# Performance work log

Hardware: AMD Instinct MI355X
Metric: run time of the kernel (lower is better)

The kernel has to match this reference:

```python
import jax, jax.numpy as jnp
import numpy as np
import math

B, T_TOK, D, H, L, V, NC, BS = 8, 511, 768, 12, 8, 512, 10, 512

PARAM_NAMES = ['tok_emb','cond_emb','type_emb','pos_emb','ln1_g','ln1_b','Wq','bq','Wk','bk','Wv','bv','Wp','bp','ln2_g','ln2_b','W1','b1','W2','b2','lnf_g','lnf_b','head_w']


def setup_inputs() -> dict:
    key = jax.random.key(0)
    ks = iter(jax.random.split(key, 40))
    def w(shape):
        return jax.random.normal(next(ks), shape, jnp.float32) * 0.02
    inp = {
        'idx': jax.random.randint(next(ks), (B, T_TOK), 0, V),
        'condition': jax.random.randint(next(ks), (B,), 0, NC + 1),
        'tok_emb': w((V, D)),
        'cond_emb': w((NC + 1, D)),
        'type_emb': w((2, D)),
        'pos_emb': w((1, BS, D)),
        'ln1_g': jnp.ones((L, D)), 'ln1_b': jnp.zeros((L, D)),
        'Wq': w((L, D, D)), 'bq': jnp.zeros((L, D)),
        'Wk': w((L, D, D)), 'bk': jnp.zeros((L, D)),
        'Wv': w((L, D, D)), 'bv': jnp.zeros((L, D)),
        'Wp': w((L, D, D)), 'bp': jnp.zeros((L, D)),
        'ln2_g': jnp.ones((L, D)), 'ln2_b': jnp.zeros((L, D)),
        'W1': w((L, D, 4 * D)), 'b1': jnp.zeros((L, 4 * D)),
        'W2': w((L, 4 * D, D)), 'b2': jnp.zeros((L, D)),
        'lnf_g': jnp.ones((D,)), 'lnf_b': jnp.zeros((D,)),
        'head_w': w((D, V)),
    }
    return inp


def _ln(x, g, b):
    m = x.mean(-1, keepdims=True)
    v = ((x - m) ** 2).mean(-1, keepdims=True)
    return (x - m) * jax.lax.rsqrt(v + 1e-5) * g + b


def _forward(idx, condition, p):
    b, t = idx.shape
    T = t + 1  # conditioning token prepended
    x = jnp.concatenate([p['cond_emb'][condition][:, None, :], p['tok_emb'][idx]], axis=1)
    type_ids = jnp.concatenate([jnp.zeros((1,), jnp.int32), jnp.ones((t,), jnp.int32)])
    x = x + p['pos_emb'][:, :T] + p['type_emb'][type_ids][None]
    dh = D // H
    causal = jnp.tril(jnp.ones((T, T), bool))

    def block(x, lp):
        ln1_g, ln1_b, Wq, bq, Wk, bk, Wv, bv, Wp, bp, ln2_g, ln2_b, W1, b1, W2, b2 = lp
        h = _ln(x, ln1_g, ln1_b)
        def heads(W, bias):
            return (h @ W + bias).reshape(b, T, H, dh).transpose(0, 2, 1, 3)  # [b,H,T,dh]
        q, k, v = heads(Wq, bq), heads(Wk, bk), heads(Wv, bv)
        att = jnp.einsum('bhqd,bhkd->bhqk', q, k) * (1.0 / math.sqrt(dh))
        att = jax.nn.softmax(jnp.where(causal, att, -jnp.inf), axis=-1)
        y = jnp.einsum('bhqk,bhkd->bhqd', att, v).transpose(0, 2, 1, 3).reshape(b, T, D)
        # NOTE: original Block applies ln1 in-place, so residual base is post-ln h
        x = h + (y @ Wp + bp)
        h2 = _ln(x, ln2_g, ln2_b)
        x = x + (jax.nn.gelu(h2 @ W1 + b1, approximate=False) @ W2 + b2)
        return x, None

    lp = (p['ln1_g'], p['ln1_b'], p['Wq'], p['bq'], p['Wk'], p['bk'], p['Wv'], p['bv'],
          p['Wp'], p['bp'], p['ln2_g'], p['ln2_b'], p['W1'], p['b1'], p['W2'], p['b2'])
    x, _ = jax.lax.scan(block, x, lp)
    logits = _ln(x, p['lnf_g'], p['lnf_b']) @ p['head_w']
    return logits[:, 1:, :]  # strip conditioning position (cond_len=1)


def reference(idx, condition, tok_emb, cond_emb, type_emb, pos_emb, ln1_g, ln1_b, Wq, bq, Wk, bk, Wv, bv, Wp, bp, ln2_g, ln2_b, W1, b1, W2, b2, lnf_g, lnf_b, head_w):
    p = dict(zip(PARAM_NAMES, (tok_emb, cond_emb, type_emb, pos_emb, ln1_g, ln1_b, Wq, bq, Wk, bk, Wv, bv, Wp, bp, ln2_g, ln2_b, W1, b1, W2, b2, lnf_g, lnf_b, head_w)))
    return _forward(idx, condition, p)
```

## Files before the change

kernel.cpp:

```cpp
#include <hip/hip_runtime.h>
#include <hip/hip_bf16.h>
#include <cstddef>
#include <cstdint>


#define NTOK 4096
#define TSEQ 512
#define DMODEL 768
#define DFF 3072
#define NHEAD 12
#define DHEAD 64
#define NLAYER 8
#define VOCAB 512
#define QKVD 2304

typedef __attribute__((ext_vector_type(8))) __bf16 bf16x8;
typedef __attribute__((ext_vector_type(4))) float f32x4;
typedef __attribute__((ext_vector_type(4))) unsigned int u32x4;
typedef __attribute__((ext_vector_type(4))) unsigned short u16x4;

__device__ __forceinline__ unsigned short f2bf(float f) {
  union { float f; unsigned int u; } v; v.f = f;
  return (unsigned short)((v.u + 0x7FFFu + ((v.u >> 16) & 1u)) >> 16);
}

__device__ __forceinline__ float gelu_exact(float x) {
  return 0.5f * x * (1.f + erff(x * 0.70710678118654752f));
}

__device__ __forceinline__ void gload_lds16(const void* g, void* lds) {
  __builtin_amdgcn_global_load_lds(
      reinterpret_cast<__attribute__((address_space(1))) void*>(
          reinterpret_cast<uintptr_t>(g)),
      reinterpret_cast<__attribute__((address_space(3))) void*>(
          reinterpret_cast<uintptr_t>(lds)),
      16, 0, 0);
}

__global__ __launch_bounds__(256) void embed_k(
    const int* __restrict__ idx, const int* __restrict__ cond,
    const float* __restrict__ tok, const float* __restrict__ ce,
    const float* __restrict__ te, const float* __restrict__ pe,
    float* __restrict__ X) {
  int row = blockIdx.x;
  int b = row >> 9, t = row & 511;
  int tid = threadIdx.x;
  const float* src = (t == 0) ? (ce + (size_t)cond[b] * DMODEL)
                              : (tok + (size_t)idx[b * 511 + t - 1] * DMODEL);
  const float* ty = te + (t != 0 ? DMODEL : 0);
  const float* pp = pe + (size_t)t * DMODEL;
  float* dst = X + (size_t)row * DMODEL;
#pragma unroll
  for (int i = 0; i < 3; i++) {
    int d = tid + i * 256;
    dst[d] = src[d] + pp[d] + ty[d];
  }
}

template <bool F32OUT>
__global__ __launch_bounds__(256) void ln_k(
    const float* __restrict__ X, const float* __restrict__ g,
    const float* __restrict__ bta, float* __restrict__ O,
    unsigned short* __restrict__ Ob) {
  const int row = blockIdx.x;
  const int tid = threadIdx.x;
  const float* x = X + (size_t)row * DMODEL;
  float v0 = x[tid], v1 = x[tid + 256], v2 = x[tid + 512];
  float s = v0 + v1 + v2;
  float ss = v0 * v0 + v1 * v1 + v2 * v2;
#pragma unroll
  for (int o = 32; o > 0; o >>= 1) {
    s += __shfl_down(s, o);
    ss += __shfl_down(ss, o);
  }
  __shared__ float sm[8];
  const int wid = tid >> 6, lane = tid & 63;
  if (lane == 0) { sm[wid] = s; sm[wid + 4] = ss; }
  __syncthreads();
  float st = sm[0] + sm[1] + sm[2] + sm[3];
  float sst = sm[4] + sm[5] + sm[6] + sm[7];
  float mean = st * (1.f / DMODEL);
  float var = sst * (1.f / DMODEL) - mean * mean;
  float rstd = rsqrtf(var + 1e-5f);
  float y0 = (v0 - mean) * rstd * g[tid] + bta[tid];
  float y1 = (v1 - mean) * rstd * g[tid + 256] + bta[tid + 256];
  float y2 = (v2 - mean) * rstd * g[tid + 512] + bta[tid + 512];
  if (F32OUT) {
    float* o = O + (size_t)row * DMODEL;
    o[tid] = y0; o[tid + 256] = y1; o[tid + 512] = y2;
  }
  unsigned short* ob = Ob + (size_t)row * DMODEL;
  ob[tid] = f2bf(y0); ob[tid + 256] = f2bf(y1); ob[tid + 512] = f2bf(y2);
}

struct P4 { const float* p[4]; };

__global__ __launch_bounds__(256) void transp_k(P4 src,
                                                unsigned short* __restrict__ out,
                                                int K, int N) {
  __shared__ float Ls[64][65];
  const float* W = src.p[blockIdx.z];
  unsigned short* o = out + (size_t)blockIdx.z * K * N;
  const int tid = threadIdx.x;
  const int n0 = blockIdx.x * 64, k0 = blockIdx.y * 64;
  const int r = tid >> 4, c4 = (tid & 15) * 4;
#pragma unroll
  for (int i = 0; i < 4; i++) {
    const int kk = r + i * 16;
    const float4 v = *(const float4*)(W + (size_t)(k0 + kk) * N + n0 + c4);
    Ls[c4 + 0][kk] = v.x;
    Ls[c4 + 1][kk] = v.y;
    Ls[c4 + 2][kk] = v.z;
    Ls[c4 + 3][kk] = v.w;
  }
  __syncthreads();
#pragma unroll
  for (int i = 0; i < 4; i++) {
    const int nn = r + i * 16;
    u16x4 q;
    q.x = f2bf(Ls[nn][c4 + 0]);
    q.y = f2bf(Ls[nn][c4 + 1]);
    q.z = f2bf(Ls[nn][c4 + 2]);
    q.w = f2bf(Ls[nn][c4 + 3]);
    *(u16x4*)(o + (size_t)(n0 + nn) * K + k0 + c4) = q;
  }
}

__global__ __launch_bounds__(256) void packb_k(const float* __restrict__ bq,
                                               const float* __restrict__ bk,
                                               const float* __restrict__ bv,
                                               float* __restrict__ o) {
  const int l = blockIdx.x, tid = threadIdx.x;
#pragma unroll
  for (int i = 0; i < 9; i++) {
    int n = tid + i * 256;
    float v = (n < 768) ? bq[l * 768 + n]
                        : (n < 1536) ? bk[l * 768 + n - 768]
                                     : bv[l * 768 + n - 1536];
    o[l * QKVD + n] = v;
  }
}

#define BK 32

constexpr int EPQ = 0;
constexpr int EPRES = 1;
constexpr int EPGELU = 2;
constexpr int EPHEAD = 3;
constexpr int EPQB = 4;

template <int EP, int TBM, int TBN>
__global__ __launch_bounds__(256) void mm_k(
    const unsigned short* __restrict__ A, const unsigned short* __restrict__ Bt,
    const float* __restrict__ bias, const float* __restrict__ res,
    void* __restrict__ Cv, int K, int N) {
  __shared__ unsigned short As[TBM * BK];
  __shared__ unsigned short Bs[TBN * BK];
  constexpr int WM = TBM / 2, WN = TBN / 2;
  constexpr int MI = WM / 16, NJ = WN / 16;
  const int tid = threadIdx.x;
  const int lane = tid & 63, wid = tid >> 6;
  const int wr = wid >> 1, wc = wid & 1;
  const int m0 = blockIdx.x * TBM, n0 = blockIdx.y * TBN;

  f32x4 acc[MI][NJ];
#pragma unroll
  for (int i = 0; i < MI; i++)
#pragma unroll
    for (int j = 0; j < NJ; j++) acc[i][j] = f32x4{0.f, 0.f, 0.f, 0.f};

  const int srow = lane >> 2;
  const int gch = (lane & 3) ^ (srow & 3);
  const size_t rb = (size_t)K * 2;
  const int fr = lane & 15, ks = lane >> 4;

  for (int k0 = 0; k0 < K; k0 += BK) {
#pragma unroll
    for (int t = 0; t < TBM / 64; t++) {
      const int rr = wid * (TBM / 4) + t * 16;
      gload_lds16((const char*)A + (size_t)(m0 + rr + srow) * rb +
                      (size_t)k0 * 2 + gch * 16,
                  As + rr * BK);
    }
#pragma unroll
    for (int t = 0; t < TBN / 64; t++) {
      const int rr = wid * (TBN / 4) + t * 16;
      gload_lds16((const char*)Bt + (size_t)(n0 + rr + srow) * rb +
                      (size_t)k0 * 2 + gch * 16,
                  Bs + rr * BK);
    }
    __syncthreads();

    u32x4 ar[MI], br[NJ];
#pragma unroll
    for (int i = 0; i < MI; i++) {
      const int ra = wr * WM + i * 16 + fr;
      ar[i] = *(const u32x4*)((const char*)As + ra * 64 + ((ks ^ (ra & 3)) << 4));
    }
#pragma unroll
    for (int j = 0; j < NJ; j++) {
      const int rbw = wc * WN + j * 16 + fr;
      br[j] = *(const u32x4*)((const char*)Bs + rbw * 64 + ((ks ^ (rbw & 3)) << 4));
    }
#pragma unroll
    for (int i = 0; i < MI; i++)
#pragma unroll
      for (int j = 0; j < NJ; j++)
        acc[i][j] = __builtin_amdgcn_mfma_f32_16x16x32_bf16(
            __builtin_bit_cast(bf16x8, ar[i]), __builtin_bit_cast(bf16x8, br[j]),
            acc[i][j], 0, 0, 0);
    __syncthreads();
  }

#pragma unroll
  for (int i = 0; i < MI; i++) {
#pragma unroll
    for (int j = 0; j < NJ; j++) {
      const int n = n0 + wc * WN + j * 16 + fr;
      float bv = 0.f;
      if (EP != EPHEAD) bv = bias[n];
#pragma unroll
      for (int r = 0; r < 4; r++) {
        const int m = m0 + wr * WM + i * 16 + ks * 4 + r;
        float v = acc[i][j][r] + bv;
        if (EP == EPRES) v += res[(size_t)m * N + n];
        if (EP == EPGELU) {
          ((unsigned short*)Cv)[(size_t)m * N + n] = f2bf(gelu_exact(v));
        } else if (EP == EPQB) {
          ((unsigned short*)Cv)[(size_t)m * N + n] = f2bf(v);
        } else if (EP == EPHEAD) {
          const int bb = m >> 9, tt = m & 511;
          if (tt)
            ((float*)Cv)[(size_t)(bb * 511 + tt - 1) * N + n] = v;
        } else {
          ((float*)Cv)[(size_t)m * N + n] = v;
        }
      }
    }
  }
}

__global__ __launch_bounds__(256) void attn_mfma_k(
    const unsigned short* __restrict__ QKV, unsigned short* __restrict__ Y) {
  __shared__ unsigned short Ks[64][72];
  __shared__ unsigned short Vt[64][72];
  __shared__ unsigned short Pl[4][16][72];
  const int qt = 7 - (int)blockIdx.x;
  const int h = blockIdx.y, b = blockIdx.z;
  const int tid = threadIdx.x;
  const int lane = tid & 63, wq = tid >> 6;
  const int fr = lane & 15, g = lane >> 4;

  const size_t qrow =
      (size_t)(b * TSEQ + qt * 64 + wq * 16 + fr) * QKVD + h * DHEAD;
  u32x4 qf[2];
  qf[0] = *(const u32x4*)(QKV + qrow + g * 8);
  qf[1] = *(const u32x4*)(QKV + qrow + 32 + g * 8);

  f32x4 of[4];
  float m[4], l[4];
#pragma unroll
  for (int jd = 0; jd < 4; jd++) of[jd] = f32x4{0.f, 0.f, 0.f, 0.f};
#pragma unroll
  for (int r = 0; r < 4; r++) { m[r] = -1e30f; l[r] = 0.f; }

  const int srow = tid >> 2, sc = (tid & 3) * 16;

  for (int kt = 0; kt <= qt; kt++) {
    {
      const size_t kr = (size_t)(b * TSEQ + kt * 64 + srow) * QKVD + h * DHEAD;
      u32x4 k0 = *(const u32x4*)(QKV + kr + DMODEL + sc);
      u32x4 k1 = *(const u32x4*)(QKV + kr + DMODEL + sc + 8);
      *(u32x4*)&Ks[srow][sc] = k0;
      *(u32x4*)&Ks[srow][sc + 8] = k1;
      u32x4 v0 = *(const u32x4*)(QKV + kr + 2 * DMODEL + sc);
      u32x4 v1 = *(const u32x4*)(QKV + kr + 2 * DMODEL + sc + 8);
      const unsigned short* vp = (const unsigned short*)&v0;
#pragma unroll
      for (int i = 0; i < 8; i++) Vt[sc + i][srow] = vp[i];
      vp = (const unsigned short*)&v1;
#pragma unroll
      for (int i = 0; i < 8; i++) Vt[sc + 8 + i][srow] = vp[i];
    }
    __syncthreads();

    f32x4 sf[4];
#pragma unroll
    for (int j = 0; j < 4; j++) sf[j] = f32x4{0.f, 0.f, 0.f, 0.f};
#pragma unroll
    for (int st = 0; st < 2; st++) {
#pragma unroll
      for (int j = 0; j < 4; j++) {
        u32x4 kf = *(const u32x4*)&Ks[j * 16 + fr][st * 32 + g * 8];
        sf[j] = __builtin_amdgcn_mfma_f32_16x16x32_bf16(
            __builtin_bit_cast(bf16x8, qf[st]), __builtin_bit_cast(bf16x8, kf),
            sf[j], 0, 0, 0);
      }
    }

    const bool diag = (kt == qt);
#pragma unroll
    for (int r = 0; r < 4; r++) {
      float pv[4];
      float mx = -1e30f;
#pragma unroll
      for (int j = 0; j < 4; j++) {
        float sv = sf[j][r] * 0.125f;
        if (diag && (j * 16 + fr > wq * 16 + g * 4 + r)) sv = -1e30f;
        pv[j] = sv;
        mx = fmaxf(mx, sv);
      }
      mx = fmaxf(mx, __shfl_xor(mx, 1));
      mx = fmaxf(mx, __shfl_xor(mx, 2));
      mx = fmaxf(mx, __shfl_xor(mx, 4));
      mx = fmaxf(mx, __shfl_xor(mx, 8));
      const float mn = fmaxf(m[r], mx);
      const float corr = __expf(m[r] - mn);
      m[r] = mn;
      float ls = 0.f;
#pragma unroll
      for (int j = 0; j < 4; j++) {
        const float e = __expf(pv[j] - mn);
        Pl[wq][g * 4 + r][j * 16 + fr] = f2bf(e);
        ls += e;
      }
      ls += __shfl_xor(ls, 1);
      ls += __shfl_xor(ls, 2);
      ls += __shfl_xor(ls, 4);
      ls += __shfl_xor(ls, 8);
      l[r] = l[r] * corr + ls;
#pragma unroll
      for (int jd = 0; jd < 4; jd++) of[jd][r] *= corr;
    }

#pragma unroll
    for (int st = 0; st < 2; st++) {
      u32x4 pf = *(const u32x4*)&Pl[wq][fr][st * 32 + g * 8];
#pragma unroll
      for (int jd = 0; jd < 4; jd++) {
        u32x4 vf = *(const u32x4*)&Vt[jd * 16 + fr][st * 32 + g * 8];
        of[jd] = __builtin_amdgcn_mfma_f32_16x16x32_bf16(
            __builtin_bit_cast(bf16x8, pf), __builtin_bit_cast(bf16x8, vf),
            of[jd], 0, 0, 0);
      }
    }
    __syncthreads();
  }

#pragma unroll
  for (int r = 0; r < 4; r++) {
    const float inv = 1.f / l[r];
    const size_t orow =
        (size_t)(b * TSEQ + qt * 64 + wq * 16 + g * 4 + r) * DMODEL + h * DHEAD;
#pragma unroll
    for (int jd = 0; jd < 4; jd++)
      Y[orow + jd * 16 + fr] = f2bf(of[jd][r] * inv);
  }
}

extern "C" void kernel_launch(void* const* d_in, const int* in_sizes, int n_in,
                              void* d_out, int out_size, void* d_ws, size_t ws_size,
                              hipStream_t stream) {
  const int* idx = (const int*)d_in[0];
  const int* condition = (const int*)d_in[1];
  const float* tok_emb = (const float*)d_in[2];
  const float* cond_emb = (const float*)d_in[3];
  const float* type_emb = (const float*)d_in[4];
  const float* pos_emb = (const float*)d_in[5];
  const float* ln1_g = (const float*)d_in[6];
  const float* ln1_b = (const float*)d_in[7];
  const float* Wq = (const float*)d_in[8];
  const float* bq = (const float*)d_in[9];
  const float* Wk = (const float*)d_in[10];
  const float* bk = (const float*)d_in[11];
  const float* Wv = (const float*)d_in[12];
  const float* bv = (const float*)d_in[13];
  const float* Wp = (const float*)d_in[14];
  const float* bp = (const float*)d_in[15];
  const float* ln2_g = (const float*)d_in[16];
  const float* ln2_b = (const float*)d_in[17];
  const float* W1 = (const float*)d_in[18];
  const float* b1 = (const float*)d_in[19];
  const float* W2 = (const float*)d_in[20];
  const float* b2 = (const float*)d_in[21];
  const float* lnf_g = (const float*)d_in[22];
  const float* lnf_b = (const float*)d_in[23];
  const float* head_w = (const float*)d_in[24];

  const size_t WDD = (size_t)DMODEL * DMODEL;
  const size_t WDF = (size_t)DMODEL * DFF;
  const size_t SD = (size_t)NTOK * DMODEL;

  char* wp = (char*)d_ws;
  auto alloc = [&](size_t bytes) {
    char* r = wp;
    wp += (bytes + 255) & ~(size_t)255;
    return r;
  };
  float* x = (float*)alloc(SD * 4);
  float* h = (float*)alloc(SD * 4);
  unsigned short* hb = (unsigned short*)alloc(SD * 2);
  unsigned short* big = (unsigned short*)alloc((size_t)NTOK * DFF * 2);
  unsigned short* qkv16 = big;
  unsigned short* m1b = big;
  unsigned short* yb = (unsigned short*)alloc(SD * 2);
  unsigned short* lw = (unsigned short*)alloc((4 * WDD + 2 * WDF) * 2);
  unsigned short* headt = (unsigned short*)alloc((size_t)VOCAB * DMODEL * 2);
  float* qkvb = (float*)alloc((size_t)NLAYER * QKVD * 4);

  unsigned short* lwQKV = lw;
  unsigned short* lwP = lw + 3 * WDD;
  unsigned short* lw1 = lw + 4 * WDD;
  unsigned short* lw2 = lw + 4 * WDD + WDF;

  embed_k<<<NTOK, 256, 0, stream>>>(idx, condition, tok_emb, cond_emb,
                                    type_emb, pos_emb, x);
  packb_k<<<NLAYER, 256, 0, stream>>>(bq, bk, bv, qkvb);
  {
    P4 s{{head_w, nullptr, nullptr, nullptr}};
    transp_k<<<dim3(VOCAB / 64, DMODEL / 64, 1), 256, 0, stream>>>(
        s, headt, DMODEL, VOCAB);
  }

  const dim3 gQKV(NTOK / 128, QKVD / 128);
  const dim3 gDD64(NTOK / 64, DMODEL / 64);
  const dim3 gDF(NTOK / 128, DFF / 128);
  const dim3 gDV(NTOK / 64, VOCAB / 64);

  for (int l = 0; l < NLAYER; l++) {
    {
      P4 s{{Wq + l * WDD, Wk + l * WDD, Wv + l * WDD, Wp + l * WDD}};
      transp_k<<<dim3(12, 12, 4), 256, 0, stream>>>(s, lw, DMODEL, DMODEL);
      P4 s1{{W1 + l * WDF, nullptr, nullptr, nullptr}};
      transp_k<<<dim3(48, 12, 1), 256, 0, stream>>>(s1, lw1, DMODEL, DFF);
      P4 s2{{W2 + l * WDF, nullptr, nullptr, nullptr}};
      transp_k<<<dim3(12, 48, 1), 256, 0, stream>>>(s2, lw2, DFF, DMODEL);
    }
    ln_k<true><<<NTOK, 256, 0, stream>>>(x, ln1_g + l * DMODEL,
                                         ln1_b + l * DMODEL, h, hb);
    mm_k<EPQB, 128, 128><<<gQKV, 256, 0, stream>>>(
        hb, lwQKV, qkvb + l * QKVD, nullptr, qkv16, DMODEL, QKVD);
    attn_mfma_k<<<dim3(8, NHEAD, 8), 256, 0, stream>>>(qkv16, yb);
    mm_k<EPRES, 64, 64><<<gDD64, 256, 0, stream>>>(
        yb, lwP, bp + l * DMODEL, h, x, DMODEL, DMODEL);
    ln_k<false><<<NTOK, 256, 0, stream>>>(x, ln2_g + l * DMODEL,
                                          ln2_b + l * DMODEL, nullptr, hb);
    mm_k<EPGELU, 128, 128><<<gDF, 256, 0, stream>>>(
        hb, lw1, b1 + l * DFF, nullptr, m1b, DMODEL, DFF);
    mm_k<EPRES, 64, 64><<<gDD64, 256, 0, stream>>>(
        m1b, lw2, b2 + l * DMODEL, x, x, DFF, DMODEL);
  }

  ln_k<false><<<NTOK, 256, 0, stream>>>(x, lnf_g, lnf_b, nullptr, hb);
  mm_k<EPHEAD, 64, 64><<<gDV, 256, 0, stream>>>(
      hb, headt, nullptr, nullptr, d_out, DMODEL, VOCAB);
}
```

Measured before the change: 1.672 ms.

## Triple-buffer GEMM LDS tiles with async prefetch and enlarge small-GEMM tiles

The GEMM kernel now keeps three LDS buffers and issues global-to-LDS loads two K-steps ahead. It waits with explicit vmcnt counts and a single barrier per step instead of two __syncthreads, so loads overlap the MFMA work. The LDS swizzle changes to XOR on row>>1, and MFMA sections get raised wave priority. The projection, FFN2 and head GEMMs switch from 64x64 to 128x64 tiles, which halves their grid size in exchange for more reuse, and this risks lower occupancy from the tripled LDS and fewer blocks.

After: 1.559 ms. 1.07x faster.

```diff
diff --git a/kernel.cpp b/kernel.cpp
--- a/kernel.cpp
+++ b/kernel.cpp
@@ -35,6 +35,15 @@
       reinterpret_cast<__attribute__((address_space(3))) void*>(
           reinterpret_cast<uintptr_t>(lds)),
       16, 0, 0);
+}
+
+template <int N>
+__device__ __forceinline__ void waitvm() {
+  if constexpr (N == 0) asm volatile("s_waitcnt vmcnt(0)" ::: "memory");
+  else if constexpr (N == 2) asm volatile("s_waitcnt vmcnt(2)" ::: "memory");
+  else if constexpr (N == 3) asm volatile("s_waitcnt vmcnt(3)" ::: "memory");
+  else if constexpr (N == 4) asm volatile("s_waitcnt vmcnt(4)" ::: "memory");
+  else static_assert(N == 0, "unsupported vmcnt");
 }
 
 __global__ __launch_bounds__(256) void embed_k(
@@ -98,7 +107,7 @@
 __global__ __launch_bounds__(256) void transp_k(P4 src,
                                                 unsigned short* __restrict__ out,
                                                 int K, int N) {
-  __shared__ float Ls[64][65];
+  __shared__ alignas(16) float Ls[64][65];
   const float* W = src.p[blockIdx.z];
   unsigned short* o = out + (size_t)blockIdx.z * K * N;
   const int tid = threadIdx.x;
@@ -154,10 +163,12 @@
     const unsigned short* __restrict__ A, const unsigned short* __restrict__ Bt,
     const float* __restrict__ bias, const float* __restrict__ res,
     void* __restrict__ Cv, int K, int N) {
-  __shared__ unsigned short As[TBM * BK];
-  __shared__ unsigned short Bs[TBN * BK];
+  __shared__ alignas(16) unsigned short As[3][TBM * BK];
+  __shared__ alignas(16) unsigned short Bs[3][TBN * BK];
   constexpr int WM = TBM / 2, WN = TBN / 2;
   constexpr int MI = WM / 16, NJ = WN / 16;
+  constexpr int GA = TBM / 64, GB = TBN / 64;
+  constexpr int G = GA + GB;
   const int tid = threadIdx.x;
   const int lane = tid & 63, wid = tid >> 6;
   const int wr = wid >> 1, wc = wid & 1;
@@ -170,38 +181,54 @@
     for (int j = 0; j < NJ; j++) acc[i][j] = f32x4{0.f, 0.f, 0.f, 0.f};
 
   const int srow = lane >> 2;
-  const int gch = (lane & 3) ^ (srow & 3);
+  const int gch = (lane & 3) ^ ((srow >> 1) & 3);
   const size_t rb = (size_t)K * 2;
   const int fr = lane & 15, ks = lane >> 4;
-
-  for (int k0 = 0; k0 < K; k0 += BK) {
-#pragma unroll
-    for (int t = 0; t < TBM / 64; t++) {
+  const int NKI = K / BK;
+
+  auto stage = [&](int kt, int slot) {
+    const size_t koff = (size_t)kt * BK * 2;
+#pragma unroll
+    for (int t = 0; t < GA; t++) {
       const int rr = wid * (TBM / 4) + t * 16;
-      gload_lds16((const char*)A + (size_t)(m0 + rr + srow) * rb +
-                      (size_t)k0 * 2 + gch * 16,
-                  As + rr * BK);
-    }
-#pragma unroll
-    for (int t = 0; t < TBN / 64; t++) {
+      gload_lds16((const char*)A + (size_t)(m0 + rr + srow) * rb + koff + gch * 16,
+                  &As[slot][rr * BK]);
+    }
+#pragma unroll
+    for (int t = 0; t < GB; t++) {
       const int rr = wid * (TBN / 4) + t * 16;
-      gload_lds16((const char*)Bt + (size_t)(n0 + rr + srow) * rb +
-                      (size_t)k0 * 2 + gch * 16,
-                  Bs + rr * BK);
-    }
-    __syncthreads();
-
+      gload_lds16((const char*)Bt + (size_t)(n0 + rr + srow) * rb + koff + gch * 16,
+                  &Bs[slot][rr * BK]);
+    }
+  };
+
+  stage(0, 0);
+  stage(1, 1);
+  waitvm<G>();
+  __builtin_amdgcn_s_barrier();
+  __builtin_amdgcn_sched_barrier(0);
+
+  int cur = 0;
+  for (int t = 0; t < NKI; ++t) {
+    const unsigned short* Ab = &As[cur][0];
+    const unsigned short* Bb = &Bs[cur][0];
     u32x4 ar[MI], br[NJ];
 #pragma unroll
     for (int i = 0; i < MI; i++) {
       const int ra = wr * WM + i * 16 + fr;
-      ar[i] = *(const u32x4*)((const char*)As + ra * 64 + ((ks ^ (ra & 3)) << 4));
+      ar[i] = *(const u32x4*)((const char*)Ab + ra * 64 +
+                              ((ks ^ ((ra >> 1) & 3)) << 4));
     }
 #pragma unroll
     for (int j = 0; j < NJ; j++) {
       const int rbw = wc * WN + j * 16 + fr;
-      br[j] = *(const u32x4*)((const char*)Bs + rbw * 64 + ((ks ^ (rbw & 3)) << 4));
-    }
+      br[j] = *(const u32x4*)((const char*)Bb + rbw * 64 +
+                              ((ks ^ ((rbw >> 1) & 3)) << 4));
+    }
+    const int nslot = (cur >= 1) ? cur - 1 : cur + 2;
+    const bool pf = (t + 2 < NKI);
+    if (pf) stage(t + 2, nslot);
+    __builtin_amdgcn_s_setprio(1);
 #pragma unroll
     for (int i = 0; i < MI; i++)
 #pragma unroll
@@ -209,7 +236,12 @@
         acc[i][j] = __builtin_amdgcn_mfma_f32_16x16x32_bf16(
             __builtin_bit_cast(bf16x8, ar[i]), __builtin_bit_cast(bf16x8, br[j]),
             acc[i][j], 0, 0, 0);
-    __syncthreads();
+    __builtin_amdgcn_s_setprio(0);
+    if (pf) waitvm<G>(); else waitvm<0>();
+    __builtin_amdgcn_sched_barrier(0);
+    __builtin_amdgcn_s_barrier();
+    __builtin_amdgcn_sched_barrier(0);
+    cur = (cur == 2) ? 0 : cur + 1;
   }
 
 #pragma unroll
@@ -242,9 +274,9 @@
 
 __global__ __launch_bounds__(256) void attn_mfma_k(
     const unsigned short* __restrict__ QKV, unsigned short* __restrict__ Y) {
-  __shared__ unsigned short Ks[64][72];
-  __shared__ unsigned short Vt[64][72];
-  __shared__ unsigned short Pl[4][16][72];
+  __shared__ alignas(16) unsigned short Ks[64][72];
+  __shared__ alignas(16) unsigned short Vt[64][72];
+  __shared__ alignas(16) unsigned short Pl[4][16][72];
   const int qt = 7 - (int)blockIdx.x;
   const int h = blockIdx.y, b = blockIdx.z;
   const int tid = threadIdx.x;
@@ -423,9 +455,9 @@
   }
 
   const dim3 gQKV(NTOK / 128, QKVD / 128);
-  const dim3 gDD64(NTOK / 64, DMODEL / 64);
+  const dim3 gDD(NTOK / 128, DMODEL / 64);
   const dim3 gDF(NTOK / 128, DFF / 128);
-  const dim3 gDV(NTOK / 64, VOCAB / 64);
+  const dim3 gDV(NTOK / 128, VOCAB / 64);
 
   for (int l = 0; l < NLAYER; l++) {
     {
@@ -441,17 +473,17 @@
     mm_k<EPQB, 128, 128><<<gQKV, 256, 0, stream>>>(
         hb, lwQKV, qkvb + l * QKVD, nullptr, qkv16, DMODEL, QKVD);
     attn_mfma_k<<<dim3(8, NHEAD, 8), 256, 0, stream>>>(qkv16, yb);
-    mm_k<EPRES, 64, 64><<<gDD64, 256, 0, stream>>>(
+    mm_k<EPRES, 128, 64><<<gDD, 256, 0, stream>>>(
         yb, lwP, bp + l * DMODEL, h, x, DMODEL, DMODEL);
     ln_k<false><<<NTOK, 256, 0, stream>>>(x, ln2_g + l * DMODEL,
                                           ln2_b + l * DMODEL, nullptr, hb);
     mm_k<EPGELU, 128, 128><<<gDF, 256, 0, stream>>>(
         hb, lw1, b1 + l * DFF, nullptr, m1b, DMODEL, DFF);
-    mm_k<EPRES, 64, 64><<<gDD64, 256, 0, stream>>>(
+    mm_k<EPRES, 128, 64><<<gDD, 256, 0, stream>>>(
         m1b, lw2, b2 + l * DMODEL, x, x, DFF, DMODEL);
   }
 
   ln_k<false><<<NTOK, 256, 0, stream>>>(x, lnf_g, lnf_b, nullptr, hb);
-  mm_k<EPHEAD, 64, 64><<<gDV, 256, 0, stream>>>(
+  mm_k<EPHEAD, 128, 64><<<gDV, 256, 0, stream>>>(
       hb, headt, nullptr, nullptr, d_out, DMODEL, VOCAB);
 }
```
